# Performance work log

Hardware: AMD Instinct MI355X
Metric: run time of the kernel (lower is better)

Reference implementation:

```python
import jax, jax.numpy as jnp
import numpy as np

N_NODES = 100000
N_EDGES = 1600000
D_FEAT = 64
COS_EPS = 1e-8  # torch.nn.functional.cosine_similarity default eps


def setup_inputs() -> dict:
    key = jax.random.key(0)
    k1, k2 = jax.random.split(key)
    features = jax.random.normal(k1, (N_NODES, D_FEAT), dtype=jnp.float32)
    edge_index = jax.random.randint(k2, (2, N_EDGES), 0, N_NODES, dtype=jnp.int64)
    return {"features": features, "edge_index": edge_index}


def _mean_agg(h, src, dst, n_nodes):
    # copy_u: message = h[src]; fn.mean: per-dst mean over incoming messages
    msg_sum = jax.ops.segment_sum(h[src], dst, num_segments=n_nodes)  # [N, d]
    deg = jax.ops.segment_sum(jnp.ones(src.shape, h.dtype), dst, num_segments=n_nodes)  # [N]
    deg = deg[:, None]
    # nodes with zero in-degree get 0 (DGL mean semantics)
    return jnp.where(deg > 0, msg_sum / jnp.maximum(deg, 1.0), 0.0)


def reference(features, edge_index):
    src, dst = edge_index[0], edge_index[1]
    n = features.shape[0]
    x1 = _mean_agg(features, src, dst, n)   # gcn1
    x2 = _mean_agg(x1, src, dst, n)         # gcn2
    # cosine similarity along feature dim
    dot = jnp.sum(x1 * x2, axis=-1)
    n1 = jnp.linalg.norm(x1, axis=-1)
    n2 = jnp.linalg.norm(x2, axis=-1)
    cos = dot / jnp.maximum(n1 * n2, COS_EPS)
    w = cos[:, None]
    return w * x2 + (1.0 - w) * x1
```

## Files before the change

### kernel.cpp

```cpp
#include <hip/hip_runtime.h>
#include <hip/hip_fp16.h>
#include <math.h>

#define N_NODES 100000
#define N_EDGES 1600000
#define D_FEAT  64

#define NPB     256
#define NBC     ((N_NODES + NPB - 1) / NPB)
#define F1_WGS  512
#define NV4     (N_EDGES / 4)
#define CHUNK_V ((NV4 + F1_WGS - 1) / F1_WGS)
#define STAGE_CAP 8192
#define CASTN   ((N_NODES * D_FEAT) / 4)
#define CAST_BLOCKS ((CASTN + 255) / 256)

#define GCAP    68


__device__ __forceinline__ uint4 pack8(const float* v) {
    __half2 h0 = __floats2half2_rn(v[0], v[1]);
    __half2 h1 = __floats2half2_rn(v[2], v[3]);
    __half2 h2 = __floats2half2_rn(v[4], v[5]);
    __half2 h3 = __floats2half2_rn(v[6], v[7]);
    uint4 st;
    st.x = *(unsigned*)&h0; st.y = *(unsigned*)&h1;
    st.z = *(unsigned*)&h2; st.w = *(unsigned*)&h3;
    return st;
}

__device__ __forceinline__ void unp8(uint4 u, float* a) {
    { __half2 h = *(__half2*)&u.x; float2 f = __half22float2(h); a[0]=f.x; a[1]=f.y; }
    { __half2 h = *(__half2*)&u.y; float2 f = __half22float2(h); a[2]=f.x; a[3]=f.y; }
    { __half2 h = *(__half2*)&u.z; float2 f = __half22float2(h); a[4]=f.x; a[5]=f.y; }
    { __half2 h = *(__half2*)&u.w; float2 f = __half22float2(h); a[6]=f.x; a[7]=f.y; }
}

__device__ __forceinline__ void acc4(uint4 u, __half2& h0, __half2& h1,
                                     __half2& h2, __half2& h3) {
    h0 = __hadd2(h0, *(__half2*)&u.x);
    h1 = __hadd2(h1, *(__half2*)&u.y);
    h2 = __hadd2(h2, *(__half2*)&u.z);
    h3 = __hadd2(h3, *(__half2*)&u.w);
}

__device__ __forceinline__ int block_excl_scan_512(int v, int t, int* wsum) {
    int lane = t & 63, wv = t >> 6;
    int incl = v;
    #pragma unroll
    for (int m = 1; m < 64; m <<= 1) {
        int o = __shfl_up(incl, m);
        if (lane >= m) incl += o;
    }
    if (lane == 63) wsum[wv] = incl;
    __syncthreads();
    int prefix = 0;
    #pragma unroll
    for (int j = 0; j < 8; j++)
        if (j < wv) prefix += wsum[j];
    return prefix + incl - v;
}


__global__ void cast_and_hist(const float* __restrict__ feat,
                              __half* __restrict__ feat_h,
                              const int4* __restrict__ dst4,
                              int* __restrict__ percnt) {
    if (blockIdx.x >= F1_WGS) {
        int i = (blockIdx.x - F1_WGS) * 256 + threadIdx.x;
        if (i < CASTN) {
            float4 v = ((const float4*)feat)[i];
            __half2 h0 = __floats2half2_rn(v.x, v.y);
            __half2 h1 = __floats2half2_rn(v.z, v.w);
            uint2 st;
            st.x = *(unsigned*)&h0;
            st.y = *(unsigned*)&h1;
            ((uint2*)feat_h)[i] = st;
        }
        return;
    }
    __shared__ int cnt[NBC];
    for (int i = threadIdx.x; i < NBC; i += blockDim.x) cnt[i] = 0;
    __syncthreads();
    int i0 = blockIdx.x * CHUNK_V;
    int i1 = min(i0 + CHUNK_V, NV4);
    for (int i = i0 + threadIdx.x; i < i1; i += blockDim.x) {
        int4 d = dst4[i];
        atomicAdd(&cnt[d.x >> 8], 1);
        atomicAdd(&cnt[d.y >> 8], 1);
        atomicAdd(&cnt[d.z >> 8], 1);
        atomicAdd(&cnt[d.w >> 8], 1);
    }
    __syncthreads();
    for (int i = threadIdx.x; i < NBC; i += blockDim.x)
        percnt[i * F1_WGS + blockIdx.x] = cnt[i];
}


__global__ __launch_bounds__(F1_WGS) void bucket_colscan(
        int* __restrict__ percnt, int* __restrict__ bhist) {
    __shared__ int wsum[8];
    int b = blockIdx.x, t = threadIdx.x;
    int v = percnt[b * F1_WGS + t];
    int excl = block_excl_scan_512(v, t, wsum);
    percnt[b * F1_WGS + t] = excl;
    if (t == F1_WGS - 1) bhist[b] = excl + v;
}

__global__ __launch_bounds__(F1_WGS) void bucketize(
        const int4* __restrict__ src4,
        const int4* __restrict__ dst4,
        const int* __restrict__ bhist,
        const int* __restrict__ percnt,
        unsigned int* __restrict__ tmp1) {
    __shared__ int base[NBC];
    __shared__ int cur[NBC];
    __shared__ int wsum[8];
    int wg = blockIdx.x, t = threadIdx.x;
    int v = (t < NBC) ? bhist[t] : 0;
    int excl = block_excl_scan_512(v, t, wsum);
    if (t < NBC) {
        base[t] = excl + percnt[t * F1_WGS + wg];
        cur[t] = 0;
    }
    __syncthreads();
    int i0 = wg * CHUNK_V;
    int i1 = min(i0 + CHUNK_V, NV4);
    for (int i = i0 + t; i < i1; i += F1_WGS) {
        int4 d = dst4[i];
        int4 s = src4[i];
        {
            int b = d.x >> 8; int r = atomicAdd(&cur[b], 1);
            tmp1[base[b] + r] = ((unsigned)s.x << 8) | (unsigned)(d.x & 255);
        }
        {
            int b = d.y >> 8; int r = atomicAdd(&cur[b], 1);
            tmp1[base[b] + r] = ((unsigned)s.y << 8) | (unsigned)(d.y & 255);
        }
        {
            int b = d.z >> 8; int r = atomicAdd(&cur[b], 1);
            tmp1[base[b] + r] = ((unsigned)s.z << 8) | (unsigned)(d.z & 255);
        }
        {
            int b = d.w >> 8; int r = atomicAdd(&cur[b], 1);
            tmp1[base[b] + r] = ((unsigned)s.w << 8) | (unsigned)(d.w & 255);
        }
    }
}

__global__ __launch_bounds__(512) void bucket_csr(
        const unsigned int* __restrict__ tmp1,
        const int* __restrict__ bhist,
        int* __restrict__ offsets,
        int* __restrict__ csr_src) {
    __shared__ int cnt[NPB];
    __shared__ int off[NPB];
    __shared__ int wsum[8];
    __shared__ int stage[STAGE_CAP];
    __shared__ int sEbase, sEcnt;
    int b = blockIdx.x, t = threadIdx.x;

    {
        int v = (t < NBC) ? bhist[t] : 0;
        int ex = block_excl_scan_512(v, t, wsum);
        if (t == b) { sEbase = ex; sEcnt = v; }
    }
    if (t < NPB) cnt[t] = 0;
    __syncthreads();
    int ebase = sEbase;
    int ecnt  = sEcnt;
    int node0 = b * NPB;

    for (int i = t; i < ecnt; i += 512)
        atomicAdd(&cnt[tmp1[ebase + i] & 255], 1);
    __syncthreads();

    int v = (t < NPB) ? cnt[t] : 0;
    int excl = block_excl_scan_512(v, t, wsum);
    if (t < NPB) {
        off[t] = excl;
        cnt[t] = 0;
        if (node0 + t < N_NODES) offsets[node0 + t] = ebase + excl;
    }
    if (b == NBC - 1 && t == 0) offsets[N_NODES] = N_EDGES;
    __syncthreads();

    if (ecnt <= STAGE_CAP) {
        for (int i = t; i < ecnt; i += 512) {
            unsigned u = tmp1[ebase + i];
            int d = (int)(u & 255);
            int r = atomicAdd(&cnt[d], 1);
            stage[off[d] + r] = (int)(u >> 8);
        }
        __syncthreads();
        for (int i = t; i < ecnt; i += 512)
            csr_src[ebase + i] = stage[i];
    } else {
        for (int i = t; i < ecnt; i += 512) {
            unsigned u = tmp1[ebase + i];
            int d = (int)(u & 255);
            int r = atomicAdd(&cnt[d], 1);
            csr_src[ebase + off[d] + r] = (int)(u >> 8);
        }
    }
}


__global__ __launch_bounds__(256) void gather1_kernel(
        const __half* __restrict__ feat_h,
        const int* __restrict__ offsets,
        const int* __restrict__ csr,
        __half* __restrict__ x1_h) {
    __shared__ int snbr[4][8][GCAP];
    int wv   = threadIdx.x >> 6;
    int lane = threadIdx.x & 63;
    int g    = lane >> 3;
    int fl   = lane & 7;
    int node = (blockIdx.x * 4 + wv) * 8 + g;

    int base = offsets[node];
    int deg  = offsets[node + 1] - base;
    int dcap = min(deg, GCAP);

    int* my = snbr[wv][g];
    for (int j = fl; j < dcap; j += 8)
        my[j] = csr[base + j];
    __builtin_amdgcn_wave_barrier();

    __half2 a0 = __float2half2_rn(0.f), a1 = a0, a2 = a0, a3 = a0;
    __half2 b0 = a0, b1 = a0, b2 = a0, b3 = a0;
    const __half* fb = feat_h + (fl << 3);
    int j = 0;
    for (; j + 4 <= dcap; j += 4) {
        int4 s = *(const int4*)&my[j];
        uint4 u0 = *(const uint4*)(fb + ((size_t)s.x << 6));
        uint4 u1 = *(const uint4*)(fb + ((size_t)s.y << 6));
        uint4 u2 = *(const uint4*)(fb + ((size_t)s.z << 6));
        uint4 u3 = *(const uint4*)(fb + ((size_t)s.w << 6));
        acc4(u0, a0, a1, a2, a3);
        acc4(u1, b0, b1, b2, b3);
        acc4(u2, a0, a1, a2, a3);
        acc4(u3, b0, b1, b2, b3);
    }
    for (; j < dcap; ++j) {
        int s = my[j];
        uint4 u = *(const uint4*)(fb + ((size_t)s << 6));
        acc4(u, a0, a1, a2, a3);
    }
    for (j = GCAP; j < deg; ++j) {
        int s = csr[base + j];
        uint4 u = *(const uint4*)(fb + ((size_t)s << 6));
        acc4(u, a0, a1, a2, a3);
    }
    a0 = __hadd2(a0, b0); a1 = __hadd2(a1, b1);
    a2 = __hadd2(a2, b2); a3 = __hadd2(a3, b3);

    float invf = (deg > 0) ? __builtin_amdgcn_rcpf((float)deg) : 0.0f;
    float r[8];
    { float2 f = __half22float2(a0); r[0]=f.x*invf; r[1]=f.y*invf; }
    { float2 f = __half22float2(a1); r[2]=f.x*invf; r[3]=f.y*invf; }
    { float2 f = __half22float2(a2); r[4]=f.x*invf; r[5]=f.y*invf; }
    { float2 f = __half22float2(a3); r[6]=f.x*invf; r[7]=f.y*invf; }
    *(uint4*)(x1_h + ((size_t)node << 6) + (fl << 3)) = pack8(r);
}

__global__ __launch_bounds__(256) void gather2_finalize_kernel(
        const __half* __restrict__ x1_h,
        const int* __restrict__ offsets,
        const int* __restrict__ csr,
        float* __restrict__ out) {
    __shared__ int snbr[4][8][GCAP];
    int wv   = threadIdx.x >> 6;
    int lane = threadIdx.x & 63;
    int g    = lane >> 3;
    int fl   = lane & 7;
    int node = (blockIdx.x * 4 + wv) * 8 + g;

    int base = offsets[node];
    int deg  = offsets[node + 1] - base;
    int dcap = min(deg, GCAP);

    int* my = snbr[wv][g];
    for (int j = fl; j < dcap; j += 8)
        my[j] = csr[base + j];
    __builtin_amdgcn_wave_barrier();

    __half2 a0 = __float2half2_rn(0.f), a1 = a0, a2 = a0, a3 = a0;
    __half2 c0 = a0, c1 = a0, c2 = a0, c3 = a0;
    const __half* fb = x1_h + (fl << 3);
    int j = 0;
    for (; j + 4 <= dcap; j += 4) {
        int4 s = *(const int4*)&my[j];
        uint4 u0 = *(const uint4*)(fb + ((size_t)s.x << 6));
        uint4 u1 = *(const uint4*)(fb + ((size_t)s.y << 6));
        uint4 u2 = *(const uint4*)(fb + ((size_t)s.z << 6));
        uint4 u3 = *(const uint4*)(fb + ((size_t)s.w << 6));
        acc4(u0, a0, a1, a2, a3);
        acc4(u1, c0, c1, c2, c3);
        acc4(u2, a0, a1, a2, a3);
        acc4(u3, c0, c1, c2, c3);
    }
    for (; j < dcap; ++j) {
        int s = my[j];
        uint4 u = *(const uint4*)(fb + ((size_t)s << 6));
        acc4(u, a0, a1, a2, a3);
    }
    for (j = GCAP; j < deg; ++j) {
        int s = csr[base + j];
        uint4 u = *(const uint4*)(fb + ((size_t)s << 6));
        acc4(u, a0, a1, a2, a3);
    }
    a0 = __hadd2(a0, c0); a1 = __hadd2(a1, c1);
    a2 = __hadd2(a2, c2); a3 = __hadd2(a3, c3);

    float invf = (deg > 0) ? __builtin_amdgcn_rcpf((float)deg) : 0.0f;
    float b[8];
    { float2 f = __half22float2(a0); b[0]=f.x*invf; b[1]=f.y*invf; }
    { float2 f = __half22float2(a1); b[2]=f.x*invf; b[3]=f.y*invf; }
    { float2 f = __half22float2(a2); b[4]=f.x*invf; b[5]=f.y*invf; }
    { float2 f = __half22float2(a3); b[6]=f.x*invf; b[7]=f.y*invf; }

    float a[8];
    uint4 ua = *(const uint4*)(x1_h + ((size_t)node << 6) + (fl << 3));
    unp8(ua, a);

    float dot = 0.f, nn1 = 0.f, nn2 = 0.f;
    #pragma unroll
    for (int t = 0; t < 8; t++) {
        dot += a[t] * b[t];
        nn1 += a[t] * a[t];
        nn2 += b[t] * b[t];
    }
    #pragma unroll
    for (int m = 1; m < 8; m <<= 1) {
        dot += __shfl_xor(dot, m);
        nn1 += __shfl_xor(nn1, m);
        nn2 += __shfl_xor(nn2, m);
    }

    float denom = fmaxf(__builtin_amdgcn_sqrtf(nn1 * nn2), 1e-8f);
    float w = dot * __builtin_amdgcn_rcpf(denom);
    float omw = 1.0f - w;

    float4 r0, r1;
    r0.x = w*b[0] + omw*a[0]; r0.y = w*b[1] + omw*a[1];
    r0.z = w*b[2] + omw*a[2]; r0.w = w*b[3] + omw*a[3];
    r1.x = w*b[4] + omw*a[4]; r1.y = w*b[5] + omw*a[5];
    r1.z = w*b[6] + omw*a[6]; r1.w = w*b[7] + omw*a[7];
    float* po = out + ((size_t)node << 6) + (fl << 3);
    *(float4*)po = r0;
    *(float4*)(po + 4) = r1;
}


extern "C" void kernel_launch(void* const* d_in, const int* in_sizes, int n_in,
                              void* d_out, int out_size, void* d_ws, size_t ws_size,
                              hipStream_t stream) {
    const float* feat = (const float*)d_in[0];
    const int*   eidx = (const int*)d_in[1];
    const int4*  src4 = (const int4*)eidx;
    const int4*  dst4 = (const int4*)(eidx + N_EDGES);

    __half*       feat_h  = (__half*)d_ws;
    __half*       x1_h    = feat_h + (size_t)N_NODES * D_FEAT;
    unsigned int* tmp1    = (unsigned int*)(x1_h + (size_t)N_NODES * D_FEAT);
    int*          csr_src = (int*)(tmp1 + N_EDGES);
    int*          offsets = csr_src + N_EDGES;
    int*          percnt  = offsets + (N_NODES + 1);
    int*          bhist   = percnt + NBC * F1_WGS;
    float*        out     = (float*)d_out;

    cast_and_hist <<<F1_WGS + CAST_BLOCKS, 256, 0, stream>>>(feat, feat_h, dst4, percnt);
    bucket_colscan<<<NBC, F1_WGS, 0, stream>>>(percnt, bhist);
    bucketize     <<<F1_WGS, F1_WGS, 0, stream>>>(src4, dst4, bhist, percnt, tmp1);
    bucket_csr    <<<NBC, 512, 0, stream>>>(tmp1, bhist, offsets, csr_src);

    int nblocks = N_NODES / 32;
    gather1_kernel<<<nblocks, 256, 0, stream>>>(feat_h, offsets, csr_src, x1_h);
    gather2_finalize_kernel<<<nblocks, 256, 0, stream>>>(x1_h, offsets, csr_src, out);
}
```

Baseline: 162.3 us.

## Halve CSR bucket width, precompute bucket bases in one scan kernel

Bucket size drops from 256 to 128 nodes, so there are about 782 buckets and twice as many blocks in bucket_csr. A new single-block kernel computes the exclusive scan of bucket counts once. Before, bucketize and every bucket_csr block re-scanned the histogram themselves, and with NBC above 512 that per-block scan would no longer fit one thread per bucket. bucket_csr now caches the raw bucket entries in shared memory, so the second pass reads LDS instead of global memory, at the cost of an extra launch and larger percnt/LDS arrays in the earlier kernels.

```diff
diff --git a/kernel.cpp b/kernel.cpp
--- a/kernel.cpp
+++ b/kernel.cpp
@@ -6,12 +6,12 @@
 #define N_EDGES 1600000
 #define D_FEAT  64
 
-#define NPB     256
+#define NPB     128
 #define NBC     ((N_NODES + NPB - 1) / NPB)
 #define F1_WGS  512
 #define NV4     (N_EDGES / 4)
 #define CHUNK_V ((NV4 + F1_WGS - 1) / F1_WGS)
-#define STAGE_CAP 8192
+#define RAW_CAP 4096
 #define CASTN   ((N_NODES * D_FEAT) / 4)
 #define CAST_BLOCKS ((CASTN + 255) / 256)
 
@@ -86,10 +86,10 @@
     int i1 = min(i0 + CHUNK_V, NV4);
     for (int i = i0 + threadIdx.x; i < i1; i += blockDim.x) {
         int4 d = dst4[i];
-        atomicAdd(&cnt[d.x >> 8], 1);
-        atomicAdd(&cnt[d.y >> 8], 1);
-        atomicAdd(&cnt[d.z >> 8], 1);
-        atomicAdd(&cnt[d.w >> 8], 1);
+        atomicAdd(&cnt[d.x >> 7], 1);
+        atomicAdd(&cnt[d.y >> 7], 1);
+        atomicAdd(&cnt[d.z >> 7], 1);
+        atomicAdd(&cnt[d.w >> 7], 1);
     }
     __syncthreads();
     for (int i = threadIdx.x; i < NBC; i += blockDim.x)
@@ -107,21 +107,31 @@
     if (t == F1_WGS - 1) bhist[b] = excl + v;
 }
 
+__global__ __launch_bounds__(512) void bucket_scan(
+        const int* __restrict__ bhist, int* __restrict__ bbase) {
+    __shared__ int wsum[8];
+    int t = threadIdx.x;
+    int i0 = 2 * t, i1 = 2 * t + 1;
+    int e0 = (i0 < NBC) ? bhist[i0] : 0;
+    int e1 = (i1 < NBC) ? bhist[i1] : 0;
+    int v = e0 + e1;
+    int excl = block_excl_scan_512(v, t, wsum);
+    if (i0 <= NBC) bbase[i0] = excl;
+    if (i1 <= NBC) bbase[i1] = excl + e0;
+}
+
 __global__ __launch_bounds__(F1_WGS) void bucketize(
         const int4* __restrict__ src4,
         const int4* __restrict__ dst4,
-        const int* __restrict__ bhist,
+        const int* __restrict__ bbase,
         const int* __restrict__ percnt,
         unsigned int* __restrict__ tmp1) {
     __shared__ int base[NBC];
     __shared__ int cur[NBC];
-    __shared__ int wsum[8];
     int wg = blockIdx.x, t = threadIdx.x;
-    int v = (t < NBC) ? bhist[t] : 0;
-    int excl = block_excl_scan_512(v, t, wsum);
-    if (t < NBC) {
-        base[t] = excl + percnt[t * F1_WGS + wg];
-        cur[t] = 0;
+    for (int i = t; i < NBC; i += F1_WGS) {
+        base[i] = bbase[i] + percnt[i * F1_WGS + wg];
+        cur[i] = 0;
     }
     __syncthreads();
     int i0 = wg * CHUNK_V;
@@ -130,49 +140,52 @@
         int4 d = dst4[i];
         int4 s = src4[i];
         {
-            int b = d.x >> 8; int r = atomicAdd(&cur[b], 1);
-            tmp1[base[b] + r] = ((unsigned)s.x << 8) | (unsigned)(d.x & 255);
+            int b = d.x >> 7; int r = atomicAdd(&cur[b], 1);
+            tmp1[base[b] + r] = ((unsigned)s.x << 7) | (unsigned)(d.x & 127);
         }
         {
-            int b = d.y >> 8; int r = atomicAdd(&cur[b], 1);
-            tmp1[base[b] + r] = ((unsigned)s.y << 8) | (unsigned)(d.y & 255);
+            int b = d.y >> 7; int r = atomicAdd(&cur[b], 1);
+            tmp1[base[b] + r] = ((unsigned)s.y << 7) | (unsigned)(d.y & 127);
         }
         {
-            int b = d.z >> 8; int r = atomicAdd(&cur[b], 1);
-            tmp1[base[b] + r] = ((unsigned)s.z << 8) | (unsigned)(d.z & 255);
+            int b = d.z >> 7; int r = atomicAdd(&cur[b], 1);
+            tmp1[base[b] + r] = ((unsigned)s.z << 7) | (unsigned)(d.z & 127);
         }
         {
-            int b = d.w >> 8; int r = atomicAdd(&cur[b], 1);
-            tmp1[base[b] + r] = ((unsigned)s.w << 8) | (unsigned)(d.w & 255);
+            int b = d.w >> 7; int r = atomicAdd(&cur[b], 1);
+            tmp1[base[b] + r] = ((unsigned)s.w << 7) | (unsigned)(d.w & 127);
         }
     }
 }
 
 __global__ __launch_bounds__(512) void bucket_csr(
         const unsigned int* __restrict__ tmp1,
-        const int* __restrict__ bhist,
+        const int* __restrict__ bbase,
         int* __restrict__ offsets,
         int* __restrict__ csr_src) {
     __shared__ int cnt[NPB];
     __shared__ int off[NPB];
     __shared__ int wsum[8];
-    __shared__ int stage[STAGE_CAP];
-    __shared__ int sEbase, sEcnt;
+    __shared__ unsigned int raw[RAW_CAP];
+    __shared__ int stage[RAW_CAP];
     int b = blockIdx.x, t = threadIdx.x;
-
-    {
-        int v = (t < NBC) ? bhist[t] : 0;
-        int ex = block_excl_scan_512(v, t, wsum);
-        if (t == b) { sEbase = ex; sEcnt = v; }
-    }
+    int ebase = bbase[b];
+    int ecnt  = bbase[b + 1] - ebase;
+    int node0 = b * NPB;
+
     if (t < NPB) cnt[t] = 0;
     __syncthreads();
-    int ebase = sEbase;
-    int ecnt  = sEcnt;
-    int node0 = b * NPB;
-
-    for (int i = t; i < ecnt; i += 512)
-        atomicAdd(&cnt[tmp1[ebase + i] & 255], 1);
+
+    if (ecnt <= RAW_CAP) {
+        for (int i = t; i < ecnt; i += 512) {
+            unsigned u = tmp1[ebase + i];
+            raw[i] = u;
+            atomicAdd(&cnt[u & 127], 1);
+        }
+    } else {
+        for (int i = t; i < ecnt; i += 512)
+            atomicAdd(&cnt[tmp1[ebase + i] & 127], 1);
+    }
     __syncthreads();
 
     int v = (t < NPB) ? cnt[t] : 0;
@@ -185,12 +198,12 @@
     if (b == NBC - 1 && t == 0) offsets[N_NODES] = N_EDGES;
     __syncthreads();
 
-    if (ecnt <= STAGE_CAP) {
+    if (ecnt <= RAW_CAP) {
         for (int i = t; i < ecnt; i += 512) {
-            unsigned u = tmp1[ebase + i];
-            int d = (int)(u & 255);
+            unsigned u = raw[i];
+            int d = (int)(u & 127);
             int r = atomicAdd(&cnt[d], 1);
-            stage[off[d] + r] = (int)(u >> 8);
+            stage[off[d] + r] = (int)(u >> 7);
         }
         __syncthreads();
         for (int i = t; i < ecnt; i += 512)
@@ -198,9 +211,9 @@
     } else {
         for (int i = t; i < ecnt; i += 512) {
             unsigned u = tmp1[ebase + i];
-            int d = (int)(u & 255);
+            int d = (int)(u & 127);
             int r = atomicAdd(&cnt[d], 1);
-            csr_src[ebase + off[d] + r] = (int)(u >> 8);
+            csr_src[ebase + off[d] + r] = (int)(u >> 7);
         }
     }
 }
@@ -368,12 +381,14 @@
     int*          offsets = csr_src + N_EDGES;
     int*          percnt  = offsets + (N_NODES + 1);
     int*          bhist   = percnt + NBC * F1_WGS;
+    int*          bbase   = bhist + NBC;
     float*        out     = (float*)d_out;
 
     cast_and_hist <<<F1_WGS + CAST_BLOCKS, 256, 0, stream>>>(feat, feat_h, dst4, percnt);
     bucket_colscan<<<NBC, F1_WGS, 0, stream>>>(percnt, bhist);
-    bucketize     <<<F1_WGS, F1_WGS, 0, stream>>>(src4, dst4, bhist, percnt, tmp1);
-    bucket_csr    <<<NBC, 512, 0, stream>>>(tmp1, bhist, offsets, csr_src);
+    bucket_scan   <<<1, 512, 0, stream>>>(bhist, bbase);
+    bucketize     <<<F1_WGS, F1_WGS, 0, stream>>>(src4, dst4, bbase, percnt, tmp1);
+    bucket_csr    <<<NBC, 512, 0, stream>>>(tmp1, bbase, offsets, csr_src);
 
     int nblocks = N_NODES / 32;
     gather1_kernel<<<nblocks, 256, 0, stream>>>(feat_h, offsets, csr_src, x1_h);
```

After: 170.1 us. 1.05x slower.

## Build CSR with global atomic per-node histogram and direct scatter

Applied to the files above, without the earlier changes.

Replaces the two-level bucket sort (per-block bucket histograms, column scan, bucketize into a temp array, per-bucket local sort) with a global-atomic per-node degree histogram, a per-bucket local scan, and a single scatter pass that uses global atomics on per-node cursors. Gather kernels now read a (start, degree) pair plus a per-bucket base instead of a flat offsets array. This removes two kernel launches and the temp array round trip. In exchange it adds a memset and heavy global atomic traffic across 1.6M edges with random scattered writes. The neighbour order within a node also becomes nondeterministic, which changes fp16 summation order.

```diff
diff --git a/kernel.cpp b/kernel.cpp
--- a/kernel.cpp
+++ b/kernel.cpp
@@ -8,12 +8,11 @@
 
 #define NPB     256
 #define NBC     ((N_NODES + NPB - 1) / NPB)
-#define F1_WGS  512
 #define NV4     (N_EDGES / 4)
-#define CHUNK_V ((NV4 + F1_WGS - 1) / F1_WGS)
-#define STAGE_CAP 8192
+#define HIST_BLOCKS ((NV4 + 255) / 256)
 #define CASTN   ((N_NODES * D_FEAT) / 4)
 #define CAST_BLOCKS ((CASTN + 255) / 256)
+#define SCAT_BLOCKS ((NV4 + 511) / 512)
 
 #define GCAP    68
 
@@ -65,150 +64,112 @@
 __global__ void cast_and_hist(const float* __restrict__ feat,
                               __half* __restrict__ feat_h,
                               const int4* __restrict__ dst4,
-                              int* __restrict__ percnt) {
-    if (blockIdx.x >= F1_WGS) {
-        int i = (blockIdx.x - F1_WGS) * 256 + threadIdx.x;
-        if (i < CASTN) {
-            float4 v = ((const float4*)feat)[i];
-            __half2 h0 = __floats2half2_rn(v.x, v.y);
-            __half2 h1 = __floats2half2_rn(v.z, v.w);
-            uint2 st;
-            st.x = *(unsigned*)&h0;
-            st.y = *(unsigned*)&h1;
-            ((uint2*)feat_h)[i] = st;
+                              int* __restrict__ ncnt) {
+    if (blockIdx.x < HIST_BLOCKS) {
+        int i = blockIdx.x * 256 + threadIdx.x;
+        if (i < NV4) {
+            int4 d = dst4[i];
+            atomicAdd(&ncnt[d.x], 1);
+            atomicAdd(&ncnt[d.y], 1);
+            atomicAdd(&ncnt[d.z], 1);
+            atomicAdd(&ncnt[d.w], 1);
         }
         return;
     }
-    __shared__ int cnt[NBC];
-    for (int i = threadIdx.x; i < NBC; i += blockDim.x) cnt[i] = 0;
+    int i = (blockIdx.x - HIST_BLOCKS) * 256 + threadIdx.x;
+    if (i < CASTN) {
+        float4 v = ((const float4*)feat)[i];
+        __half2 h0 = __floats2half2_rn(v.x, v.y);
+        __half2 h1 = __floats2half2_rn(v.z, v.w);
+        uint2 st;
+        st.x = *(unsigned*)&h0;
+        st.y = *(unsigned*)&h1;
+        ((uint2*)feat_h)[i] = st;
+    }
+}
+
+
+__global__ __launch_bounds__(NPB) void bucket_local(
+        const int* __restrict__ ncnt,
+        int2* __restrict__ nodinfo,
+        int* __restrict__ ncur,
+        int* __restrict__ btot) {
+    __shared__ int wsum[4];
+    int b = blockIdx.x, t = threadIdx.x;
+    int node = b * NPB + t;
+    int deg = (node < N_NODES) ? ncnt[node] : 0;
+    int lane = t & 63, wv = t >> 6;
+    int incl = deg;
+    #pragma unroll
+    for (int m = 1; m < 64; m <<= 1) {
+        int o = __shfl_up(incl, m);
+        if (lane >= m) incl += o;
+    }
+    if (lane == 63) wsum[wv] = incl;
     __syncthreads();
-    int i0 = blockIdx.x * CHUNK_V;
-    int i1 = min(i0 + CHUNK_V, NV4);
-    for (int i = i0 + threadIdx.x; i < i1; i += blockDim.x) {
-        int4 d = dst4[i];
-        atomicAdd(&cnt[d.x >> 8], 1);
-        atomicAdd(&cnt[d.y >> 8], 1);
-        atomicAdd(&cnt[d.z >> 8], 1);
-        atomicAdd(&cnt[d.w >> 8], 1);
-    }
-    __syncthreads();
-    for (int i = threadIdx.x; i < NBC; i += blockDim.x)
-        percnt[i * F1_WGS + blockIdx.x] = cnt[i];
-}
-
-
-__global__ __launch_bounds__(F1_WGS) void bucket_colscan(
-        int* __restrict__ percnt, int* __restrict__ bhist) {
-    __shared__ int wsum[8];
-    int b = blockIdx.x, t = threadIdx.x;
-    int v = percnt[b * F1_WGS + t];
-    int excl = block_excl_scan_512(v, t, wsum);
-    percnt[b * F1_WGS + t] = excl;
-    if (t == F1_WGS - 1) bhist[b] = excl + v;
-}
-
-__global__ __launch_bounds__(F1_WGS) void bucketize(
+    int prefix = 0;
+    #pragma unroll
+    for (int j = 0; j < 4; j++)
+        if (j < wv) prefix += wsum[j];
+    int excl = prefix + incl - deg;
+    if (node < N_NODES) {
+        nodinfo[node] = make_int2(excl, deg);
+        ncur[node] = 0;
+    }
+    if (t == NPB - 1) btot[b] = excl + deg;
+}
+
+
+__global__ __launch_bounds__(512) void scatter_csr(
         const int4* __restrict__ src4,
         const int4* __restrict__ dst4,
-        const int* __restrict__ bhist,
-        const int* __restrict__ percnt,
-        unsigned int* __restrict__ tmp1) {
-    __shared__ int base[NBC];
-    __shared__ int cur[NBC];
+        const int2* __restrict__ nodinfo,
+        const int* __restrict__ btot,
+        int* __restrict__ bbase,
+        int* __restrict__ ncur,
+        int* __restrict__ csr) {
+    __shared__ int sbase[NBC];
     __shared__ int wsum[8];
-    int wg = blockIdx.x, t = threadIdx.x;
-    int v = (t < NBC) ? bhist[t] : 0;
+    int t = threadIdx.x;
+    int v = (t < NBC) ? btot[t] : 0;
     int excl = block_excl_scan_512(v, t, wsum);
     if (t < NBC) {
-        base[t] = excl + percnt[t * F1_WGS + wg];
-        cur[t] = 0;
+        sbase[t] = excl;
+        if (blockIdx.x == 0) bbase[t] = excl;
     }
     __syncthreads();
-    int i0 = wg * CHUNK_V;
-    int i1 = min(i0 + CHUNK_V, NV4);
-    for (int i = i0 + t; i < i1; i += F1_WGS) {
-        int4 d = dst4[i];
-        int4 s = src4[i];
-        {
-            int b = d.x >> 8; int r = atomicAdd(&cur[b], 1);
-            tmp1[base[b] + r] = ((unsigned)s.x << 8) | (unsigned)(d.x & 255);
-        }
-        {
-            int b = d.y >> 8; int r = atomicAdd(&cur[b], 1);
-            tmp1[base[b] + r] = ((unsigned)s.y << 8) | (unsigned)(d.y & 255);
-        }
-        {
-            int b = d.z >> 8; int r = atomicAdd(&cur[b], 1);
-            tmp1[base[b] + r] = ((unsigned)s.z << 8) | (unsigned)(d.z & 255);
-        }
-        {
-            int b = d.w >> 8; int r = atomicAdd(&cur[b], 1);
-            tmp1[base[b] + r] = ((unsigned)s.w << 8) | (unsigned)(d.w & 255);
-        }
-    }
-}
-
-__global__ __launch_bounds__(512) void bucket_csr(
-        const unsigned int* __restrict__ tmp1,
-        const int* __restrict__ bhist,
-        int* __restrict__ offsets,
-        int* __restrict__ csr_src) {
-    __shared__ int cnt[NPB];
-    __shared__ int off[NPB];
-    __shared__ int wsum[8];
-    __shared__ int stage[STAGE_CAP];
-    __shared__ int sEbase, sEcnt;
-    int b = blockIdx.x, t = threadIdx.x;
-
+
+    int i = blockIdx.x * 512 + t;
+    if (i >= NV4) return;
+    int4 d = dst4[i];
+    int4 s = src4[i];
     {
-        int v = (t < NBC) ? bhist[t] : 0;
-        int ex = block_excl_scan_512(v, t, wsum);
-        if (t == b) { sEbase = ex; sEcnt = v; }
-    }
-    if (t < NPB) cnt[t] = 0;
-    __syncthreads();
-    int ebase = sEbase;
-    int ecnt  = sEcnt;
-    int node0 = b * NPB;
-
-    for (int i = t; i < ecnt; i += 512)
-        atomicAdd(&cnt[tmp1[ebase + i] & 255], 1);
-    __syncthreads();
-
-    int v = (t < NPB) ? cnt[t] : 0;
-    int excl = block_excl_scan_512(v, t, wsum);
-    if (t < NPB) {
-        off[t] = excl;
-        cnt[t] = 0;
-        if (node0 + t < N_NODES) offsets[node0 + t] = ebase + excl;
-    }
-    if (b == NBC - 1 && t == 0) offsets[N_NODES] = N_EDGES;
-    __syncthreads();
-
-    if (ecnt <= STAGE_CAP) {
-        for (int i = t; i < ecnt; i += 512) {
-            unsigned u = tmp1[ebase + i];
-            int d = (int)(u & 255);
-            int r = atomicAdd(&cnt[d], 1);
-            stage[off[d] + r] = (int)(u >> 8);
-        }
-        __syncthreads();
-        for (int i = t; i < ecnt; i += 512)
-            csr_src[ebase + i] = stage[i];
-    } else {
-        for (int i = t; i < ecnt; i += 512) {
-            unsigned u = tmp1[ebase + i];
-            int d = (int)(u & 255);
-            int r = atomicAdd(&cnt[d], 1);
-            csr_src[ebase + off[d] + r] = (int)(u >> 8);
-        }
+        int2 ni = nodinfo[d.x];
+        int r = atomicAdd(&ncur[d.x], 1);
+        csr[sbase[d.x >> 8] + ni.x + r] = s.x;
+    }
+    {
+        int2 ni = nodinfo[d.y];
+        int r = atomicAdd(&ncur[d.y], 1);
+        csr[sbase[d.y >> 8] + ni.x + r] = s.y;
+    }
+    {
+        int2 ni = nodinfo[d.z];
+        int r = atomicAdd(&ncur[d.z], 1);
+        csr[sbase[d.z >> 8] + ni.x + r] = s.z;
+    }
+    {
+        int2 ni = nodinfo[d.w];
+        int r = atomicAdd(&ncur[d.w], 1);
+        csr[sbase[d.w >> 8] + ni.x + r] = s.w;
     }
 }
 
 
 __global__ __launch_bounds__(256) void gather1_kernel(
         const __half* __restrict__ feat_h,
-        const int* __restrict__ offsets,
+        const int2* __restrict__ nodinfo,
+        const int* __restrict__ bbase,
         const int* __restrict__ csr,
         __half* __restrict__ x1_h) {
     __shared__ int snbr[4][8][GCAP];
@@ -218,8 +179,9 @@
     int fl   = lane & 7;
     int node = (blockIdx.x * 4 + wv) * 8 + g;
 
-    int base = offsets[node];
-    int deg  = offsets[node + 1] - base;
+    int2 ni  = nodinfo[node];
+    int base = bbase[node >> 8] + ni.x;
+    int deg  = ni.y;
     int dcap = min(deg, GCAP);
 
     int* my = snbr[wv][g];
@@ -266,7 +228,8 @@
 
 __global__ __launch_bounds__(256) void gather2_finalize_kernel(
         const __half* __restrict__ x1_h,
-        const int* __restrict__ offsets,
+        const int2* __restrict__ nodinfo,
+        const int* __restrict__ bbase,
         const int* __restrict__ csr,
         float* __restrict__ out) {
     __shared__ int snbr[4][8][GCAP];
@@ -276,8 +239,9 @@
     int fl   = lane & 7;
     int node = (blockIdx.x * 4 + wv) * 8 + g;
 
-    int base = offsets[node];
-    int deg  = offsets[node + 1] - base;
+    int2 ni  = nodinfo[node];
+    int base = bbase[node >> 8] + ni.x;
+    int deg  = ni.y;
     int dcap = min(deg, GCAP);
 
     int* my = snbr[wv][g];
@@ -361,21 +325,25 @@
     const int4*  src4 = (const int4*)eidx;
     const int4*  dst4 = (const int4*)(eidx + N_EDGES);
 
-    __half*       feat_h  = (__half*)d_ws;
-    __half*       x1_h    = feat_h + (size_t)N_NODES * D_FEAT;
-    unsigned int* tmp1    = (unsigned int*)(x1_h + (size_t)N_NODES * D_FEAT);
-    int*          csr_src = (int*)(tmp1 + N_EDGES);
-    int*          offsets = csr_src + N_EDGES;
-    int*          percnt  = offsets + (N_NODES + 1);
-    int*          bhist   = percnt + NBC * F1_WGS;
-    float*        out     = (float*)d_out;
-
-    cast_and_hist <<<F1_WGS + CAST_BLOCKS, 256, 0, stream>>>(feat, feat_h, dst4, percnt);
-    bucket_colscan<<<NBC, F1_WGS, 0, stream>>>(percnt, bhist);
-    bucketize     <<<F1_WGS, F1_WGS, 0, stream>>>(src4, dst4, bhist, percnt, tmp1);
-    bucket_csr    <<<NBC, 512, 0, stream>>>(tmp1, bhist, offsets, csr_src);
+    __half* feat_h  = (__half*)d_ws;
+    __half* x1_h    = feat_h + (size_t)N_NODES * D_FEAT;
+    int*    csr     = (int*)(x1_h + (size_t)N_NODES * D_FEAT);
+    int*    ncnt    = csr + N_EDGES;
+    int*    ncur    = ncnt + N_NODES;
+    int2*   nodinfo = (int2*)(ncur + N_NODES);
+    int*    btot    = (int*)(nodinfo + N_NODES);
+    int*    bbase   = btot + NBC;
+    float*  out     = (float*)d_out;
+
+    hipMemsetAsync(ncnt, 0, N_NODES * sizeof(int), stream);
+
+    cast_and_hist<<<HIST_BLOCKS + CAST_BLOCKS, 256, 0, stream>>>(
+        feat, feat_h, dst4, ncnt);
+    bucket_local<<<NBC, NPB, 0, stream>>>(ncnt, nodinfo, ncur, btot);
+    scatter_csr<<<SCAT_BLOCKS, 512, 0, stream>>>(
+        src4, dst4, nodinfo, btot, bbase, ncur, csr);
 
     int nblocks = N_NODES / 32;
-    gather1_kernel<<<nblocks, 256, 0, stream>>>(feat_h, offsets, csr_src, x1_h);
-    gather2_finalize_kernel<<<nblocks, 256, 0, stream>>>(x1_h, offsets, csr_src, out);
-}
+    gather1_kernel<<<nblocks, 256, 0, stream>>>(feat_h, nodinfo, bbase, csr, x1_h);
+    gather2_finalize_kernel<<<nblocks, 256, 0, stream>>>(x1_h, nodinfo, bbase, csr, out);
+}
```

Measured after the change: 293.7 us. +80.9%, slower.
